# Kernel optimization log

Hardware: AMD Instinct MI355X
Metric: run time of the kernel (lower is better)

Reference implementation:

```python
import jax, jax.numpy as jnp
import numpy as np

B, S, D = 8, 1024, 768
H, DK, DV = 12, 64, 64
NEG = -1e12


def setup_inputs() -> dict:
    key = jax.random.key(0)
    ks = jax.random.split(key, 8)
    s = 0.02
    return {
        "x": jax.random.normal(ks[0], (B, S, D), jnp.float32),
        "Wq": jax.random.normal(ks[1], (D, H * DK), jnp.float32) * s,
        "bq": jnp.zeros((H * DK,), jnp.float32),
        "Wk": jax.random.normal(ks[2], (D, H * DK), jnp.float32) * s,
        "bk": jnp.zeros((H * DK,), jnp.float32),
        "Wv": jax.random.normal(ks[3], (D, H * DV), jnp.float32) * s,
        "bv": jnp.zeros((H * DV,), jnp.float32),
        "Wo": jax.random.normal(ks[4], (H * DV, D), jnp.float32) * s,
        "bo": jnp.zeros((D,), jnp.float32),
        "position_bias": jax.random.normal(ks[5], (S, S, DK), jnp.float32) * s,
        "q_mask": jnp.ones((B, S), jnp.float32),
        "v_mask": jnp.ones((B, S), jnp.float32),
    }


def reference(x, Wq, bq, Wk, bk, Wv, bv, Wo, bo, position_bias, q_mask, v_mask):
    b, s, _ = x.shape
    qw = (x @ Wq + bq).reshape(b, s, H, DK)  # [b,s,h,dk]
    kw = (x @ Wk + bk).reshape(b, s, H, DK)
    vw = (x @ Wv + bv).reshape(b, s, H, DV)
    # scores with fused typical_relative position bias
    a = jnp.einsum("bjhd,bkhd->bhjk", qw, kw)
    a = a + jnp.einsum("bjhd,jkd->bhjk", qw, position_bias)
    a = a / jnp.sqrt(jnp.float32(DK))
    # mask keys (v_mask): additive -1e12 on padded positions
    a = a + (1.0 - v_mask)[:, None, None, :] * NEG
    A = jax.nn.softmax(a, axis=-1)
    o = jnp.einsum("bhjk,bkhd->bjhd", A, vw)
    o = o + jnp.einsum("bhjk,jkd->bjhd", A, position_bias)
    o = o.reshape(b, s, H * DV)
    o = o @ Wo + bo
    # zero out padded query positions (q_mask, multiplicative)
    o = o * q_mask[:, :, None]
    return o
```

## Files before the change

### kernel.cpp

```cpp
#include <hip/hip_runtime.h>

#define B_  8
#define S_  1024
#define D_  768
#define H_  12
#define DK_ 64
#define BH_ 96

typedef _Float16 f16;
typedef _Float16 f16x8 __attribute__((ext_vector_type(8)));
typedef _Float16 f16x4 __attribute__((ext_vector_type(4)));
typedef float    f32x4 __attribute__((ext_vector_type(4)));

#define MFMA16(a, b, c) __builtin_amdgcn_mfma_f32_16x16x32_f16((a), (b), (c), 0, 0, 0)

__device__ __forceinline__ int swz(int row) { return ((row ^ (row >> 3)) & 7) << 4; }

__device__ __forceinline__ f16x8 lds_read8(const f16* base, int row, int rowbytes, int colbyte) {
    const char* p = (const char*)base + row * rowbytes + (colbyte ^ swz(row));
    return *(const f16x8*)p;
}
__device__ __forceinline__ void lds_write8(f16* base, int row, int rowbytes, int colbyte, f16x8 v) {
    char* p = (char*)base + row * rowbytes + (colbyte ^ swz(row));
    *(f16x8*)p = v;
}
__device__ __forceinline__ void lds_write4(f16* base, int row, int rowbytes, int colbyte, f16x4 v) {
    char* p = (char*)base + row * rowbytes + (colbyte ^ swz(row));
    *(f16x4*)p = v;
}
__device__ __forceinline__ void lds_write1(f16* base, int row, int rowbytes, int colbyte, f16 v) {
    char* p = (char*)base + row * rowbytes + (colbyte ^ swz(row));
    *(f16*)p = v;
}
__device__ __forceinline__ f16 lds_read1(const f16* base, int row, int rowbytes, int colbyte) {
    const char* p = (const char*)base + row * rowbytes + (colbyte ^ swz(row));
    return *(const f16*)p;
}


__global__ __launch_bounds__(256) void cvt_x(const float* __restrict__ in,
                                             f16* __restrict__ out, int n4)
{
    const int i = blockIdx.x * 256 + threadIdx.x;
    if (i < n4) {
        const float4 v = ((const float4*)in)[i];
        f16x4 h; h[0] = (f16)v.x; h[1] = (f16)v.y; h[2] = (f16)v.z; h[3] = (f16)v.w;
        ((f16x4*)out)[i] = h;
    }
}

__global__ __launch_bounds__(256) void wT_cvt(
    const float* __restrict__ Wq, const float* __restrict__ Wk,
    const float* __restrict__ Wv, const float* __restrict__ Wo,
    f16* __restrict__ Tq, f16* __restrict__ Tk,
    f16* __restrict__ Tv, f16* __restrict__ To)
{
    const float* W; f16* T;
    if      (blockIdx.z == 0) { W = Wq; T = Tq; }
    else if (blockIdx.z == 1) { W = Wk; T = Tk; }
    else if (blockIdx.z == 2) { W = Wv; T = Tv; }
    else                      { W = Wo; T = To; }

    const int r0 = blockIdx.x * 32;
    const int c0 = blockIdx.y * 32;
    const int t = threadIdx.x, tx = t & 31, ty = t >> 5;

    __shared__ float tile[32][33];
    #pragma unroll
    for (int i = 0; i < 4; ++i)
        tile[ty + 8 * i][tx] = W[(size_t)(r0 + ty + 8 * i) * D_ + c0 + tx];
    __syncthreads();
    #pragma unroll
    for (int i = 0; i < 4; ++i)
        T[(size_t)(c0 + ty + 8 * i) * D_ + r0 + tx] = (f16)tile[tx][ty + 8 * i];
}

__global__ __launch_bounds__(256) void qkv_mfma(
    const f16* __restrict__ x16,
    const f16* __restrict__ Tq, const f16* __restrict__ Tk, const f16* __restrict__ Tv,
    const float* __restrict__ bq, const float* __restrict__ bk, const float* __restrict__ bv,
    f16* __restrict__ qo, f16* __restrict__ ko, f16* __restrict__ vo)
{
    const f16* WT; const float* bias; f16* out; float scale;
    if      (blockIdx.z == 0) { WT = Tq; bias = bq; out = qo; scale = 0.125f; }
    else if (blockIdx.z == 1) { WT = Tk; bias = bk; out = ko; scale = 1.0f; }
    else                      { WT = Tv; bias = bv; out = vo; scale = 1.0f; }

    const int row0 = blockIdx.x * 128;
    const int col0 = blockIdx.y * 128;
    const int t = threadIdx.x, l = t & 63, w = t >> 6;
    const int wr = w >> 1, wc = w & 1;

    __shared__ __attribute__((aligned(16))) f16 As[128 * 64];
    __shared__ __attribute__((aligned(16))) f16 Bs[128 * 64];

    f32x4 acc[4][4] = {};

    for (int kt = 0; kt < D_; kt += 64) {
        __syncthreads();
        #pragma unroll
        for (int ii = 0; ii < 4; ++ii) {
            const int idx = t + ii * 256;
            const int r = idx >> 3, c8 = idx & 7;
            f16x8 v = *(const f16x8*)(x16 + (size_t)(row0 + r) * D_ + kt + c8 * 8);
            lds_write8(As, r, 128, c8 * 16, v);
        }
        #pragma unroll
        for (int ii = 0; ii < 4; ++ii) {
            const int idx = t + ii * 256;
            const int r = idx >> 3, c8 = idx & 7;
            f16x8 v = *(const f16x8*)(WT + (size_t)(col0 + r) * D_ + kt + c8 * 8);
            lds_write8(Bs, r, 128, c8 * 16, v);
        }
        __syncthreads();
        #pragma unroll
        for (int ks = 0; ks < 2; ++ks) {
            f16x8 af[4], bf[4];
            #pragma unroll
            for (int mi = 0; mi < 4; ++mi)
                af[mi] = lds_read8(As, wr * 64 + mi * 16 + (l & 15), 128, ks * 64 + (l >> 4) * 16);
            #pragma unroll
            for (int ni = 0; ni < 4; ++ni)
                bf[ni] = lds_read8(Bs, wc * 64 + ni * 16 + (l & 15), 128, ks * 64 + (l >> 4) * 16);
            #pragma unroll
            for (int mi = 0; mi < 4; ++mi)
                #pragma unroll
                for (int ni = 0; ni < 4; ++ni)
                    acc[mi][ni] = MFMA16(af[mi], bf[ni], acc[mi][ni]);
        }
    }

    #pragma unroll
    for (int mi = 0; mi < 4; ++mi)
        #pragma unroll
        for (int q = 0; q < 4; ++q) {
            const int row = row0 + wr * 64 + mi * 16 + (l >> 4) * 4 + q;
            const int b = row >> 10, s = row & 1023;
            #pragma unroll
            for (int ni = 0; ni < 4; ++ni) {
                const int col = col0 + wc * 64 + ni * 16 + (l & 15);
                const int h = col >> 6, dk = col & 63;
                out[(((size_t)(b * H_ + h)) * S_ + s) * DK_ + dk] = (f16)((acc[mi][ni][q] + bias[col]) * scale);
            }
        }
}

__global__ __launch_bounds__(256) void vT_cvt(const f16* __restrict__ V, f16* __restrict__ Vt)
{
    const int bh = blockIdx.x;
    const int s0 = blockIdx.y * 64;
    const int t = threadIdx.x;
    __shared__ __attribute__((aligned(16))) f16 tile[64 * 64];
    #pragma unroll
    for (int ii = 0; ii < 2; ++ii) {
        const int u = t + ii * 256;
        const int r = u >> 3, c8 = u & 7;
        f16x8 v = *(const f16x8*)(V + ((size_t)bh * S_ + s0 + r) * DK_ + c8 * 8);
        lds_write8(tile, r, 128, c8 * 16, v);
    }
    __syncthreads();
    #pragma unroll
    for (int ii = 0; ii < 2; ++ii) {
        const int u = t + ii * 256;
        const int d = u >> 3, sc = u & 7;
        f16x8 o;
        #pragma unroll
        for (int e = 0; e < 8; ++e) o[e] = lds_read1(tile, sc * 8 + e, 128, d * 2);
        *(f16x8*)(Vt + ((size_t)bh * DK_ + d) * S_ + s0 + sc * 8) = o;
    }
}

__global__ __launch_bounds__(256) void s2_gemm(
    const f16* __restrict__ Qb, const float* __restrict__ pb,
    f16* __restrict__ S2, f16* __restrict__ pbT)
{
    const int j  = blockIdx.x;
    const int n0 = blockIdx.y * 256;
    const int t = threadIdx.x, l = t & 63, w = t >> 6;

    __shared__ __attribute__((aligned(16))) f16 Ps[256 * 64];

    for (int idx = t; idx < 256 * 16; idx += 256) {
        const int r = idx >> 4, c4 = idx & 15;
        const float4 v = *(const float4*)(pb + ((size_t)j * S_ + n0 + r) * DK_ + c4 * 4);
        f16x4 h; h[0] = (f16)v.x; h[1] = (f16)v.y; h[2] = (f16)v.z; h[3] = (f16)v.w;
        lds_write4(Ps, r, 128, c4 * 8, h);
    }

    f16x8 qf[6][2];
    #pragma unroll
    for (int mi = 0; mi < 6; ++mi)
        #pragma unroll
        for (int ks = 0; ks < 2; ++ks)
            qf[mi][ks] = *(const f16x8*)(Qb + ((size_t)(mi * 16 + (l & 15)) * S_ + j) * DK_ + ks * 32 + (l >> 4) * 8);

    __syncthreads();

    f32x4 acc[6][4] = {};
    #pragma unroll
    for (int s = 0; s < 4; ++s) {
        const int nrow = w * 64 + s * 16 + (l & 15);
        const f16x8 b0 = lds_read8(Ps, nrow, 128, (l >> 4) * 16);
        const f16x8 b1 = lds_read8(Ps, nrow, 128, 64 + (l >> 4) * 16);
        #pragma unroll
        for (int mi = 0; mi < 6; ++mi) {
            acc[mi][s] = MFMA16(qf[mi][0], b0, acc[mi][s]);
            acc[mi][s] = MFMA16(qf[mi][1], b1, acc[mi][s]);
        }
    }

    #pragma unroll
    for (int mi = 0; mi < 6; ++mi)
        #pragma unroll
        for (int q = 0; q < 4; ++q) {
            const int bh = mi * 16 + (l >> 4) * 4 + q;
            const size_t base = ((size_t)bh << 20) + (size_t)j * S_;
            #pragma unroll
            for (int s = 0; s < 4; ++s) {
                const int k = n0 + w * 64 + s * 16 + (l & 15);
                S2[base + k] = (f16)acc[mi][s][q];
            }
        }

    #pragma unroll
    for (int ii = 0; ii < 8; ++ii) {
        const int u = t + ii * 256;
        const int d = u >> 5, kc = u & 31;
        f16x8 o;
        #pragma unroll
        for (int e = 0; e < 8; ++e) o[e] = lds_read1(Ps, kc * 8 + e, 128, d * 2);
        *(f16x8*)(pbT + ((size_t)j * DK_ + d) * S_ + n0 + kc * 8) = o;
    }
}

__global__ __launch_bounds__(256) void attn_sm(
    const f16* __restrict__ Qb, const f16* __restrict__ Kb,
    const float* __restrict__ vmask, f16* __restrict__ S2A)
{
    const int j0 = blockIdx.x * 16;
    const int bh = blockIdx.y, b = bh / H_;
    const int t = threadIdx.x, l = t & 63, w = t >> 6;

    __shared__ __attribute__((aligned(16))) f16 SA[16 * 1024];
    __shared__ f16 mflag[1024];
    __shared__ float redm[4][16], reds[4][16];

    for (int idx = t; idx < 16 * 128; idx += 256) {
        const int r = idx >> 7, c8 = idx & 127;
        f16x8 v = *(const f16x8*)(S2A + ((size_t)bh << 20) + (size_t)(j0 + r) * S_ + c8 * 8);
        lds_write8(SA, r, 2048, c8 * 16, v);
    }
    for (int k = t; k < 1024; k += 256)
        mflag[k] = (f16)(1.0f - vmask[(size_t)b * S_ + k]);

    const f16x8 aq0 = *(const f16x8*)(Qb + ((size_t)bh * S_ + j0 + (l & 15)) * DK_ + (l >> 4) * 8);
    const f16x8 aq1 = *(const f16x8*)(Qb + ((size_t)bh * S_ + j0 + (l & 15)) * DK_ + 32 + (l >> 4) * 8);
    __syncthreads();

    f32x4 acc[16] = {};
    #pragma unroll
    for (int f = 0; f < 16; ++f) {
        const int k = (f >> 1) * 128 + w * 32 + (f & 1) * 16 + (l & 15);
        const f16* kp = Kb + ((size_t)bh * S_ + k) * DK_ + (l >> 4) * 8;
        const f16x8 b0 = *(const f16x8*)kp;
        const f16x8 b1 = *(const f16x8*)(kp + 32);
        acc[f] = MFMA16(aq0, b0, acc[f]);
        acc[f] = MFMA16(aq1, b1, acc[f]);
    }

    float mrow[4] = {-3e38f, -3e38f, -3e38f, -3e38f};
    #pragma unroll
    for (int f = 0; f < 16; ++f) {
        const int k = (f >> 1) * 128 + w * 32 + (f & 1) * 16 + (l & 15);
        const float vm = (float)mflag[k] * -30000.0f;
        #pragma unroll
        for (int q = 0; q < 4; ++q) {
            const int r = (l >> 4) * 4 + q;
            const float s2v = (float)lds_read1(SA, r, 2048, k * 2);
            const float val = acc[f][q] + s2v + vm;
            acc[f][q] = val;
            mrow[q] = fmaxf(mrow[q], val);
        }
    }
    #pragma unroll
    for (int q = 0; q < 4; ++q) {
        float m = mrow[q];
        #pragma unroll
        for (int off = 1; off < 16; off <<= 1) m = fmaxf(m, __shfl_xor(m, off));
        mrow[q] = m;
    }
    if ((l & 15) == 0) {
        #pragma unroll
        for (int q = 0; q < 4; ++q) redm[w][(l >> 4) * 4 + q] = mrow[q];
    }
    __syncthreads();
    #pragma unroll
    for (int q = 0; q < 4; ++q) {
        const int r = (l >> 4) * 4 + q;
        mrow[q] = fmaxf(fmaxf(redm[0][r], redm[1][r]), fmaxf(redm[2][r], redm[3][r]));
    }

    float lsum[4] = {0.f, 0.f, 0.f, 0.f};
    #pragma unroll
    for (int f = 0; f < 16; ++f)
        #pragma unroll
        for (int q = 0; q < 4; ++q) {
            const float e = __expf(acc[f][q] - mrow[q]);
            acc[f][q] = e;
            lsum[q] += e;
        }
    #pragma unroll
    for (int q = 0; q < 4; ++q) {
        float s = lsum[q];
        #pragma unroll
        for (int off = 1; off < 16; off <<= 1) s += __shfl_xor(s, off);
        lsum[q] = s;
    }
    if ((l & 15) == 0) {
        #pragma unroll
        for (int q = 0; q < 4; ++q) reds[w][(l >> 4) * 4 + q] = lsum[q];
    }
    __syncthreads();
    #pragma unroll
    for (int q = 0; q < 4; ++q) {
        const int r = (l >> 4) * 4 + q;
        lsum[q] = 1.0f / (reds[0][r] + reds[1][r] + reds[2][r] + reds[3][r]);
    }

    const size_t fbase = ((size_t)bh << 20) + ((size_t)(j0 >> 4) << 14) + l;
    #pragma unroll
    for (int f = 0; f < 16; ++f)
        #pragma unroll
        for (int q = 0; q < 4; ++q)
            S2A[fbase + (size_t)(((w * 16 + f) * 4 + q) * 64)] = (f16)(acc[f][q] * lsum[q]);
}

__global__ __launch_bounds__(256) void av_gemm(
    const f16* __restrict__ A, const f16* __restrict__ Vt,
    float* __restrict__ omid)
{
    const int j0 = blockIdx.x * 64;
    const int bh = blockIdx.y, b = bh / H_, h = bh % H_;
    const int t = threadIdx.x, l = t & 63, w = t >> 6;

    const int jt   = (j0 >> 4) + w;
    const int qj   = l & 3;
    const int rh   = (l & 15) >> 2;
    const int k0lo = ((l >> 4) & 1) * 8;
    const int fhi  = l >> 5;

    const f16* abase = A + ((size_t)bh << 20) + ((size_t)jt << 14) + rh * 16 + k0lo;
    const f16* vbase = Vt + (size_t)bh * DK_ * S_ + (size_t)(l & 15) * S_ + (l >> 4) * 8;

    f32x4 acc[4] = {};
    #pragma unroll 4
    for (int ks = 0; ks < 32; ++ks) {
        const int ff = 2 * (ks >> 2) + fhi;
        const f16x8 af = *(const f16x8*)(abase + (size_t)((((ks & 3) * 16 + ff) * 4 + qj) * 64));
        #pragma unroll
        for (int ni = 0; ni < 4; ++ni) {
            const f16x8 vf = *(const f16x8*)(vbase + (size_t)(ni * 16) * S_ + ks * 32);
            acc[ni] = MFMA16(af, vf, acc[ni]);
        }
    }

    #pragma unroll
    for (int ni = 0; ni < 4; ++ni)
        #pragma unroll
        for (int q = 0; q < 4; ++q) {
            const int j = j0 + w * 16 + (l >> 4) * 4 + q;
            const int d = ni * 16 + (l & 15);
            omid[((size_t)b * S_ + j) * D_ + h * DK_ + d] = acc[ni][q];
        }
}

__global__ __launch_bounds__(256) void apb_gemm(
    const f16* __restrict__ A, const f16* __restrict__ pbT,
    const float* __restrict__ omid, f16* __restrict__ omid16)
{
    const int j = blockIdx.x;
    const int t = threadIdx.x, l = t & 63, w = t >> 6;

    const int qj   = j & 3;
    const int rh   = (j >> 2) & 3;
    const int k0lo = ((l >> 4) & 1) * 8;
    const int fhi  = l >> 5;

    const f16* abase = A + ((size_t)(j >> 4) << 14) + rh * 16 + k0lo;
    const f16* bbase = pbT + ((size_t)j * DK_ + w * 16 + (l & 15)) * S_ + (l >> 4) * 8;

    f32x4 acc[6] = {};
    #pragma unroll 4
    for (int ks = 0; ks < 32; ++ks) {
        const int ff = 2 * (ks >> 2) + fhi;
        const size_t koff = (size_t)((((ks & 3) * 16 + ff) * 4 + qj) * 64);
        const f16x8 bf = *(const f16x8*)(bbase + ks * 32);
        #pragma unroll
        for (int mi = 0; mi < 6; ++mi) {
            const f16x8 af = *(const f16x8*)(abase + ((size_t)(mi * 16 + (l & 15)) << 20) + koff);
            acc[mi] = MFMA16(af, bf, acc[mi]);
        }
    }

    #pragma unroll
    for (int mi = 0; mi < 6; ++mi)
        #pragma unroll
        for (int q = 0; q < 4; ++q) {
            const int bh = mi * 16 + (l >> 4) * 4 + q;
            const int b = bh / H_, h = bh % H_;
            const int d = w * 16 + (l & 15);
            const size_t o = ((size_t)b * S_ + j) * D_ + h * DK_ + d;
            omid16[o] = (f16)(omid[o] + acc[mi][q]);
        }
}

__global__ __launch_bounds__(256) void out_mfma(
    const f16* __restrict__ a16, const f16* __restrict__ WT,
    const float* __restrict__ bias, const float* __restrict__ qm,
    float* __restrict__ out)
{
    const int row0 = blockIdx.x * 128;
    const int col0 = blockIdx.y * 128;
    const int t = threadIdx.x, l = t & 63, w = t >> 6;
    const int wr = w >> 1, wc = w & 1;

    __shared__ __attribute__((aligned(16))) f16 As[128 * 64];
    __shared__ __attribute__((aligned(16))) f16 Bs[128 * 64];

    f32x4 acc[4][4] = {};

    for (int kt = 0; kt < D_; kt += 64) {
        __syncthreads();
        #pragma unroll
        for (int ii = 0; ii < 4; ++ii) {
            const int idx = t + ii * 256;
            const int r = idx >> 3, c8 = idx & 7;
            f16x8 v = *(const f16x8*)(a16 + (size_t)(row0 + r) * D_ + kt + c8 * 8);
            lds_write8(As, r, 128, c8 * 16, v);
        }
        #pragma unroll
        for (int ii = 0; ii < 4; ++ii) {
            const int idx = t + ii * 256;
            const int r = idx >> 3, c8 = idx & 7;
            f16x8 v = *(const f16x8*)(WT + (size_t)(col0 + r) * D_ + kt + c8 * 8);
            lds_write8(Bs, r, 128, c8 * 16, v);
        }
        __syncthreads();
        #pragma unroll
        for (int ks = 0; ks < 2; ++ks) {
            f16x8 af[4], bf[4];
            #pragma unroll
            for (int mi = 0; mi < 4; ++mi)
                af[mi] = lds_read8(As, wr * 64 + mi * 16 + (l & 15), 128, ks * 64 + (l >> 4) * 16);
            #pragma unroll
            for (int ni = 0; ni < 4; ++ni)
                bf[ni] = lds_read8(Bs, wc * 64 + ni * 16 + (l & 15), 128, ks * 64 + (l >> 4) * 16);
            #pragma unroll
            for (int mi = 0; mi < 4; ++mi)
                #pragma unroll
                for (int ni = 0; ni < 4; ++ni)
                    acc[mi][ni] = MFMA16(af[mi], bf[ni], acc[mi][ni]);
        }
    }

    #pragma unroll
    for (int mi = 0; mi < 4; ++mi)
        #pragma unroll
        for (int q = 0; q < 4; ++q) {
            const int row = row0 + wr * 64 + mi * 16 + (l >> 4) * 4 + q;
            const float qmv = qm[row];
            #pragma unroll
            for (int ni = 0; ni < 4; ++ni) {
                const int col = col0 + wc * 64 + ni * 16 + (l & 15);
                out[(size_t)row * D_ + col] = (acc[mi][ni][q] + bias[col]) * qmv;
            }
        }
}

extern "C" void kernel_launch(void* const* d_in, const int* in_sizes, int n_in,
                              void* d_out, int out_size, void* d_ws, size_t ws_size,
                              hipStream_t stream) {
    const float* x  = (const float*)d_in[0];
    const float* Wq = (const float*)d_in[1];
    const float* bq = (const float*)d_in[2];
    const float* Wk = (const float*)d_in[3];
    const float* bk = (const float*)d_in[4];
    const float* Wv = (const float*)d_in[5];
    const float* bv = (const float*)d_in[6];
    const float* Wo = (const float*)d_in[7];
    const float* bo = (const float*)d_in[8];
    const float* pb = (const float*)d_in[9];
    const float* qm = (const float*)d_in[10];
    const float* vm = (const float*)d_in[11];
    float* out = (float*)d_out;

    const size_t NQ = (size_t)BH_ * S_ * DK_;
    const size_t NW = (size_t)D_ * D_;
    f16* qb  = (f16*)d_ws;
    f16* kb  = qb + NQ;
    f16* vb  = kb + NQ;
    f16* vt  = vb + NQ;
    f16* s2  = vt + NQ;
    f16* pbT = s2 + (size_t)BH_ * S_ * S_;
    f16* x16 = pbT + (size_t)S_ * DK_ * S_;
    f16* tq  = x16 + (size_t)B_ * S_ * D_;
    f16* tk  = tq + NW;
    f16* tv  = tk + NW;
    f16* to  = tv + NW;
    f16* omid16 = to + NW;
    float* omid = (float*)(omid16 + (size_t)B_ * S_ * D_);

    cvt_x<<<dim3((B_ * S_ * D_ / 4 + 255) / 256), 256, 0, stream>>>(x, x16, B_ * S_ * D_ / 4);
    wT_cvt<<<dim3(24, 24, 4), 256, 0, stream>>>(Wq, Wk, Wv, Wo, tq, tk, tv, to);

    qkv_mfma<<<dim3(64, 6, 3), 256, 0, stream>>>(x16, tq, tk, tv, bq, bk, bv, qb, kb, vb);
    vT_cvt<<<dim3(96, 16), 256, 0, stream>>>(vb, vt);

    s2_gemm <<<dim3(1024, 4), 256, 0, stream>>>(qb, pb, s2, pbT);
    attn_sm <<<dim3(64, 96),  256, 0, stream>>>(qb, kb, vm, s2);
    av_gemm <<<dim3(16, 96),  256, 0, stream>>>(s2, vt, omid);
    apb_gemm<<<dim3(1024),    256, 0, stream>>>(s2, pbT, omid, omid16);

    out_mfma<<<dim3(64, 6), 256, 0, stream>>>(omid16, to, bo, qm, out);
}
```

Baseline: 743.1 us.

## Merge four query rows per apb_gemm block with 512 threads and remapped block order

apb_gemm now gives each 512-thread block four query rows (same qj, all four rh) instead of one row per 256-thread block. Each wave computes two rows, so the A-operand fragments for neighbouring rh values are read by the same block and can share cache lines. A block-index swizzle spreads consecutive blocks across jt groups. In exchange there are fewer blocks (256) and twice the accumulator registers per thread, which could lower occupancy.

```diff
diff --git a/kernel.cpp b/kernel.cpp
--- a/kernel.cpp
+++ b/kernel.cpp
@@ -374,44 +374,58 @@
         }
 }
 
-__global__ __launch_bounds__(256) void apb_gemm(
+__global__ __launch_bounds__(512) void apb_gemm(
     const f16* __restrict__ A, const f16* __restrict__ pbT,
     const float* __restrict__ omid, f16* __restrict__ omid16)
 {
-    const int j = blockIdx.x;
+    const int bid = blockIdx.x;
+    const int g   = (bid & 7) * 32 + (bid >> 3);
+    const int jt  = g >> 2, qj = g & 3;
     const int t = threadIdx.x, l = t & 63, w = t >> 6;
-
-    const int qj   = j & 3;
-    const int rh   = (j >> 2) & 3;
+    const int dq = w & 3;
+    const int jp = w >> 2;
+
     const int k0lo = ((l >> 4) & 1) * 8;
     const int fhi  = l >> 5;
 
-    const f16* abase = A + ((size_t)(j >> 4) << 14) + rh * 16 + k0lo;
-    const f16* bbase = pbT + ((size_t)j * DK_ + w * 16 + (l & 15)) * S_ + (l >> 4) * 8;
-
-    f32x4 acc[6] = {};
-    #pragma unroll 4
+    const f16* abase = A + ((size_t)jt << 14) + k0lo;
+    const f16* bb[2];
+    #pragma unroll
+    for (int rr = 0; rr < 2; ++rr) {
+        const int j = jt * 16 + (2 * jp + rr) * 4 + qj;
+        bb[rr] = pbT + ((size_t)j * DK_ + dq * 16 + (l & 15)) * S_ + (l >> 4) * 8;
+    }
+
+    f32x4 acc[2][6] = {};
     for (int ks = 0; ks < 32; ++ks) {
         const int ff = 2 * (ks >> 2) + fhi;
         const size_t koff = (size_t)((((ks & 3) * 16 + ff) * 4 + qj) * 64);
-        const f16x8 bf = *(const f16x8*)(bbase + ks * 32);
-        #pragma unroll
-        for (int mi = 0; mi < 6; ++mi) {
-            const f16x8 af = *(const f16x8*)(abase + ((size_t)(mi * 16 + (l & 15)) << 20) + koff);
-            acc[mi] = MFMA16(af, bf, acc[mi]);
-        }
-    }
-
-    #pragma unroll
-    for (int mi = 0; mi < 6; ++mi)
-        #pragma unroll
-        for (int q = 0; q < 4; ++q) {
-            const int bh = mi * 16 + (l >> 4) * 4 + q;
-            const int b = bh / H_, h = bh % H_;
-            const int d = w * 16 + (l & 15);
-            const size_t o = ((size_t)b * S_ + j) * D_ + h * DK_ + d;
-            omid16[o] = (f16)(omid[o] + acc[mi][q]);
-        }
+        #pragma unroll
+        for (int rr = 0; rr < 2; ++rr) {
+            const int rh = 2 * jp + rr;
+            const f16x8 bf = *(const f16x8*)(bb[rr] + ks * 32);
+            #pragma unroll
+            for (int mi = 0; mi < 6; ++mi) {
+                const f16x8 af = *(const f16x8*)(abase + ((size_t)(mi * 16 + (l & 15)) << 20) + koff + rh * 16);
+                acc[rr][mi] = MFMA16(af, bf, acc[rr][mi]);
+            }
+        }
+    }
+
+    #pragma unroll
+    for (int rr = 0; rr < 2; ++rr) {
+        const int j = jt * 16 + (2 * jp + rr) * 4 + qj;
+        #pragma unroll
+        for (int mi = 0; mi < 6; ++mi)
+            #pragma unroll
+            for (int q = 0; q < 4; ++q) {
+                const int bh = mi * 16 + (l >> 4) * 4 + q;
+                const int b = bh / H_, h = bh % H_;
+                const int d = dq * 16 + (l & 15);
+                const size_t o = ((size_t)b * S_ + j) * D_ + h * DK_ + d;
+                omid16[o] = (f16)(omid[o] + acc[rr][mi][q]);
+            }
+    }
 }
 
 __global__ __launch_bounds__(256) void out_mfma(
@@ -519,7 +533,7 @@
     s2_gemm <<<dim3(1024, 4), 256, 0, stream>>>(qb, pb, s2, pbT);
     attn_sm <<<dim3(64, 96),  256, 0, stream>>>(qb, kb, vm, s2);
     av_gemm <<<dim3(16, 96),  256, 0, stream>>>(s2, vt, omid);
-    apb_gemm<<<dim3(1024),    256, 0, stream>>>(s2, pbT, omid, omid16);
+    apb_gemm<<<dim3(256),     512, 0, stream>>>(s2, pbT, omid, omid16);
 
     out_mfma<<<dim3(64, 6), 256, 0, stream>>>(omid16, to, bo, qm, out);
 }
```

Measured after the change: 804.1 us. +8.2%, slower.

## Add apb-friendly A4 and pbT4 layouts so apb_gemm reads contiguous fragments

Applied to the files above, without the earlier changes.

attn_sm now writes the softmax probabilities twice: once in the existing fragment layout for av_gemm and once in a new per-query-row A4 layout that groups all 96 heads for each key group of 8. s2_gemm writes the transposed position bias in a matching 8-wide blocked layout. apb_gemm then loads both operands with contiguous 16-byte vector reads instead of strided gathers across 1MB head planes. attn_sm's block index is remapped so neighbouring blocks share query tiles across heads. The cost is an extra 192MB-scale workspace buffer and doubled probability writes with a scattered store pattern.

```diff
diff --git a/kernel.cpp b/kernel.cpp
--- a/kernel.cpp
+++ b/kernel.cpp
@@ -172,7 +172,7 @@
 
 __global__ __launch_bounds__(256) void s2_gemm(
     const f16* __restrict__ Qb, const float* __restrict__ pb,
-    f16* __restrict__ S2, f16* __restrict__ pbT)
+    f16* __restrict__ S2, f16* __restrict__ pbT4)
 {
     const int j  = blockIdx.x;
     const int n0 = blockIdx.y * 256;
@@ -229,16 +229,21 @@
         f16x8 o;
         #pragma unroll
         for (int e = 0; e < 8; ++e) o[e] = lds_read1(Ps, kc * 8 + e, 128, d * 2);
-        *(f16x8*)(pbT + ((size_t)j * DK_ + d) * S_ + n0 + kc * 8) = o;
+        *(f16x8*)(pbT4 + (size_t)j * 65536 + ((size_t)((n0 >> 3) + kc) * 64 + d) * 8) = o;
     }
 }
 
 __global__ __launch_bounds__(256) void attn_sm(
     const f16* __restrict__ Qb, const f16* __restrict__ Kb,
-    const float* __restrict__ vmask, f16* __restrict__ S2A)
-{
-    const int j0 = blockIdx.x * 16;
-    const int bh = blockIdx.y, b = bh / H_;
+    const float* __restrict__ vmask, f16* __restrict__ S2A, f16* __restrict__ A4)
+{
+    const int bid = blockIdx.x;
+    const int c = bid & 7, m = (bid >> 3) & 7;
+    const int g = (bid >> 6) * 8 + c;
+    const int jt = g / 12;
+    const int bh = (g % 12) * 8 + m;
+    const int j0 = jt * 16;
+    const int b  = bh / H_;
     const int t = threadIdx.x, l = t & 63, w = t >> 6;
 
     __shared__ __attribute__((aligned(16))) f16 SA[16 * 1024];
@@ -284,10 +289,10 @@
     }
     #pragma unroll
     for (int q = 0; q < 4; ++q) {
-        float m = mrow[q];
-        #pragma unroll
-        for (int off = 1; off < 16; off <<= 1) m = fmaxf(m, __shfl_xor(m, off));
-        mrow[q] = m;
+        float m2 = mrow[q];
+        #pragma unroll
+        for (int off = 1; off < 16; off <<= 1) m2 = fmaxf(m2, __shfl_xor(m2, off));
+        mrow[q] = m2;
     }
     if ((l & 15) == 0) {
         #pragma unroll
@@ -327,12 +332,18 @@
         lsum[q] = 1.0f / (reds[0][r] + reds[1][r] + reds[2][r] + reds[3][r]);
     }
 
-    const size_t fbase = ((size_t)bh << 20) + ((size_t)(j0 >> 4) << 14) + l;
-    #pragma unroll
-    for (int f = 0; f < 16; ++f)
-        #pragma unroll
-        for (int q = 0; q < 4; ++q)
-            S2A[fbase + (size_t)(((w * 16 + f) * 4 + q) * 64)] = (f16)(acc[f][q] * lsum[q]);
+    const size_t fbase = ((size_t)bh << 20) + ((size_t)jt << 14) + l;
+    #pragma unroll
+    for (int f = 0; f < 16; ++f) {
+        const int kg0 = (f >> 1) * 16 + w * 4 + (f & 1) * 2 + ((l >> 3) & 1);
+        #pragma unroll
+        for (int q = 0; q < 4; ++q) {
+            const f16 a = (f16)(acc[f][q] * lsum[q]);
+            S2A[fbase + (size_t)(((w * 16 + f) * 4 + q) * 64)] = a;
+            const int j = j0 + (l >> 4) * 4 + q;
+            A4[(((size_t)j * 128 + kg0) * 96 + bh) * 8 + (l & 7)] = a;
+        }
+    }
 }
 
 __global__ __launch_bounds__(256) void av_gemm(
@@ -375,29 +386,23 @@
 }
 
 __global__ __launch_bounds__(256) void apb_gemm(
-    const f16* __restrict__ A, const f16* __restrict__ pbT,
+    const f16* __restrict__ A4, const f16* __restrict__ pbT4,
     const float* __restrict__ omid, f16* __restrict__ omid16)
 {
     const int j = blockIdx.x;
-    const int t = threadIdx.x, l = t & 63, w = t >> 6;
-
-    const int qj   = j & 3;
-    const int rh   = (j >> 2) & 3;
-    const int k0lo = ((l >> 4) & 1) * 8;
-    const int fhi  = l >> 5;
-
-    const f16* abase = A + ((size_t)(j >> 4) << 14) + rh * 16 + k0lo;
-    const f16* bbase = pbT + ((size_t)j * DK_ + w * 16 + (l & 15)) * S_ + (l >> 4) * 8;
+    const int t = threadIdx.x, l = t & 63, dq = t >> 6;
+
+    const f16* a4 = A4 + (size_t)j * (128 * 96 * 8);
+    const f16* p4 = pbT4 + (size_t)j * 65536;
 
     f32x4 acc[6] = {};
     #pragma unroll 4
     for (int ks = 0; ks < 32; ++ks) {
-        const int ff = 2 * (ks >> 2) + fhi;
-        const size_t koff = (size_t)((((ks & 3) * 16 + ff) * 4 + qj) * 64);
-        const f16x8 bf = *(const f16x8*)(bbase + ks * 32);
+        const int kg = ks * 4 + (l >> 4);
+        const f16x8 bf = *(const f16x8*)(p4 + ((size_t)kg * 64 + dq * 16 + (l & 15)) * 8);
         #pragma unroll
         for (int mi = 0; mi < 6; ++mi) {
-            const f16x8 af = *(const f16x8*)(abase + ((size_t)(mi * 16 + (l & 15)) << 20) + koff);
+            const f16x8 af = *(const f16x8*)(a4 + ((size_t)kg * 96 + mi * 16 + (l & 15)) * 8);
             acc[mi] = MFMA16(af, bf, acc[mi]);
         }
     }
@@ -408,7 +413,7 @@
         for (int q = 0; q < 4; ++q) {
             const int bh = mi * 16 + (l >> 4) * 4 + q;
             const int b = bh / H_, h = bh % H_;
-            const int d = w * 16 + (l & 15);
+            const int d = dq * 16 + (l & 15);
             const size_t o = ((size_t)b * S_ + j) * D_ + h * DK_ + d;
             omid16[o] = (f16)(omid[o] + acc[mi][q]);
         }
@@ -496,17 +501,18 @@
 
     const size_t NQ = (size_t)BH_ * S_ * DK_;
     const size_t NW = (size_t)D_ * D_;
-    f16* qb  = (f16*)d_ws;
-    f16* kb  = qb + NQ;
-    f16* vb  = kb + NQ;
-    f16* vt  = vb + NQ;
-    f16* s2  = vt + NQ;
-    f16* pbT = s2 + (size_t)BH_ * S_ * S_;
-    f16* x16 = pbT + (size_t)S_ * DK_ * S_;
-    f16* tq  = x16 + (size_t)B_ * S_ * D_;
-    f16* tk  = tq + NW;
-    f16* tv  = tk + NW;
-    f16* to  = tv + NW;
+    f16* qb   = (f16*)d_ws;
+    f16* kb   = qb + NQ;
+    f16* vb   = kb + NQ;
+    f16* vt   = vb + NQ;
+    f16* s2   = vt + NQ;
+    f16* a4   = s2 + (size_t)BH_ * S_ * S_;
+    f16* pbT4 = a4 + (size_t)BH_ * S_ * S_;
+    f16* x16  = pbT4 + (size_t)S_ * DK_ * S_;
+    f16* tq   = x16 + (size_t)B_ * S_ * D_;
+    f16* tk   = tq + NW;
+    f16* tv   = tk + NW;
+    f16* to   = tv + NW;
     f16* omid16 = to + NW;
     float* omid = (float*)(omid16 + (size_t)B_ * S_ * D_);
 
@@ -516,10 +522,10 @@
     qkv_mfma<<<dim3(64, 6, 3), 256, 0, stream>>>(x16, tq, tk, tv, bq, bk, bv, qb, kb, vb);
     vT_cvt<<<dim3(96, 16), 256, 0, stream>>>(vb, vt);
 
-    s2_gemm <<<dim3(1024, 4), 256, 0, stream>>>(qb, pb, s2, pbT);
-    attn_sm <<<dim3(64, 96),  256, 0, stream>>>(qb, kb, vm, s2);
+    s2_gemm <<<dim3(1024, 4), 256, 0, stream>>>(qb, pb, s2, pbT4);
+    attn_sm <<<dim3(6144),    256, 0, stream>>>(qb, kb, vm, s2, a4);
     av_gemm <<<dim3(16, 96),  256, 0, stream>>>(s2, vt, omid);
-    apb_gemm<<<dim3(1024),    256, 0, stream>>>(s2, pbT, omid, omid16);
+    apb_gemm<<<dim3(1024),    256, 0, stream>>>(a4, pbT4, omid, omid16);
 
     out_mfma<<<dim3(64, 6), 256, 0, stream>>>(omid16, to, bo, qm, out);
 }
```

Result: slower. 768.3 us (+3.4%).
